# Kernel optimization log

Hardware: AMD Instinct MI355X
Metric: run time of the kernel (lower is better)

The kernel has to match this reference:

```python
import jax, jax.numpy as jnp
import numpy as np

IN_DIM, DIM_MSA, PAIR_DIM = 256, 32, 64
B, L = 1, 512


def setup_inputs() -> dict:
    key = jax.random.key(0)
    k0, k1, k2, k3, k4 = jax.random.split(key, 5)
    seq_rep = jax.random.normal(k0, (B, L, IN_DIM), dtype=jnp.float32)
    # torch nn.Linear params: weight [out, in], bias [out]
    s1 = 1.0 / np.sqrt(IN_DIM)
    W1 = jax.random.uniform(k1, (DIM_MSA, IN_DIM), jnp.float32, -s1, s1)
    b1 = jax.random.uniform(k2, (DIM_MSA,), jnp.float32, -s1, s1)
    s2 = 1.0 / np.sqrt(DIM_MSA * DIM_MSA)
    W2 = jax.random.uniform(k3, (PAIR_DIM, DIM_MSA * DIM_MSA), jnp.float32, -s2, s2)
    b2 = jax.random.uniform(k4, (PAIR_DIM,), jnp.float32, -s2, s2)
    return {"seq_rep": seq_rep, "W1": W1, "b1": b1, "W2": W2, "b2": b2}


def reference(seq_rep, W1, b1, W2, b2):
    # proj_down1: [B,L,in_dim] -> [B,L,dim_msa]
    x = seq_rep @ W1.T + b1
    # outer product: 'bid,bjc -> bijcd' then flatten (c d)
    # [B,L(i),L(j),c(dim_msa),d(dim_msa)]
    outer = jnp.einsum('bid,bjc->bijcd', x, x)
    Bb, Li, Lj = outer.shape[:3]
    outer = outer.reshape(Bb, Li, Lj, DIM_MSA * DIM_MSA)  # (c d), c-major
    # proj_down2: -> [B,L,L,pairwise_dim]
    return outer @ W2.T + b2
```

## Files before the change

### kernel.cpp

```cpp
#include <hip/hip_runtime.h>


static constexpr int LL  = 512;
static constexpr int IND = 256;
static constexpr int DM  = 32;
static constexpr int PD  = 64;

typedef _Float16 f16x4 __attribute__((ext_vector_type(4)));
typedef _Float16 f16x8 __attribute__((ext_vector_type(8)));
typedef float    f32x16 __attribute__((ext_vector_type(16)));

#define LGKM_BARRIER() do { \
    asm volatile("s_waitcnt lgkmcnt(0)" ::: "memory"); \
    __builtin_amdgcn_s_barrier(); \
  } while (0)

__device__ __forceinline__ f16x4 cvt4(const float4 v) {
  f16x4 r;
  r[0] = (_Float16)v.x; r[1] = (_Float16)v.y;
  r[2] = (_Float16)v.z; r[3] = (_Float16)v.w;
  return r;
}

static constexpr int SP = 264;
static constexpr int XP = 40;

__global__ __launch_bounds__(256) void k_front(const float* __restrict__ seq,
                                               const float* __restrict__ W1,
                                               const float* __restrict__ b1,
                                               const float* __restrict__ W2,
                                               _Float16* __restrict__ xgh,
                                               _Float16* __restrict__ Ygh) {
  __shared__ __align__(16) _Float16 seqs[64 * SP];
  __shared__ __align__(16) _Float16 w1s[32 * SP];
  __shared__ __align__(16) _Float16 w2h[64 * XP];
  __shared__ __align__(16) _Float16 xh[64 * XP];
  const int c     = blockIdx.x & 31;
  const int ibase = (blockIdx.x >> 5) * 64;
  const int t     = threadIdx.x;

#pragma unroll
  for (int k = 0; k < 16; ++k) {
    const int f = t + k * 256;
    const int row = f >> 6, c4 = f & 63;
    const float4 v = *(const float4*)(seq + (size_t)(ibase + row) * IND + c4 * 4);
    *(f16x4*)&seqs[row * SP + c4 * 4] = cvt4(v);
  }
#pragma unroll
  for (int k = 0; k < 8; ++k) {
    const int f = t + k * 256;
    const int row = f >> 6, c4 = f & 63;
    const float4 v = *(const float4*)(W1 + (size_t)row * IND + c4 * 4);
    *(f16x4*)&w1s[row * SP + c4 * 4] = cvt4(v);
  }
#pragma unroll
  for (int k = 0; k < 2; ++k) {
    const int idx = t + k * 256;
    const int p = idx >> 3, d4 = idx & 7;
    const float4 v = *(const float4*)(W2 + (size_t)p * (DM * DM) + c * DM + d4 * 4);
    *(f16x4*)&w2h[p * XP + d4 * 4] = cvt4(v);
  }
  __syncthreads();

  const int w = t >> 6, lane = t & 63, l31 = lane & 31, lh = lane >> 5;

  if (w < 2) {
    const _Float16* arow = &seqs[(w * 32 + l31) * SP + lh * 8];
    const _Float16* brow = &w1s[l31 * SP + lh * 8];
    f32x16 acc = {};
#pragma unroll
    for (int ks = 0; ks < 16; ++ks) {
      const f16x8 af = *(const f16x8*)(arow + ks * 16);
      const f16x8 bf = *(const f16x8*)(brow + ks * 16);
      acc = __builtin_amdgcn_mfma_f32_32x32x16_f16(af, bf, acc, 0, 0, 0);
    }
    const float bias1 = b1[l31];
#pragma unroll
    for (int r = 0; r < 16; ++r) {
      const int mrow = w * 32 + (r & 3) + 8 * (r >> 2) + 4 * lh;
      const float v = acc[r] + bias1;
      xh[mrow * XP + l31] = (_Float16)v;
      if (c == 0) xgh[(size_t)(ibase + mrow) * DM + l31] = (_Float16)v;
    }
  }
  __syncthreads();

  {
    const int ih = w >> 1, ph = w & 1;
    const _Float16* arow = &xh[(ih * 32 + l31) * XP + lh * 8];
    const _Float16* brow = &w2h[(ph * 32 + l31) * XP + lh * 8];
    f32x16 acc = {};
    {
      const f16x8 a0 = *(const f16x8*)(arow);
      const f16x8 b0 = *(const f16x8*)(brow);
      acc = __builtin_amdgcn_mfma_f32_32x32x16_f16(a0, b0, acc, 0, 0, 0);
      const f16x8 a1 = *(const f16x8*)(arow + 16);
      const f16x8 b1 = *(const f16x8*)(brow + 16);
      acc = __builtin_amdgcn_mfma_f32_32x32x16_f16(a1, b1, acc, 0, 0, 0);
    }
    _Float16* ybase = Ygh + ((size_t)ibase * DM + c) * PD + ph * 32 + l31;
#pragma unroll
    for (int r = 0; r < 16; ++r) {
      const int irow = ih * 32 + (r & 3) + 8 * (r >> 2) + 4 * lh;
      ybase[(size_t)irow * (DM * PD)] = (_Float16)acc[r];
    }
  }
}

static constexpr int XPAD = 40;

__global__ __launch_bounds__(128, 3) void k_outer(const _Float16* __restrict__ xgh,
                                                  const _Float16* __restrict__ Ygh,
                                                  const float* __restrict__ b2,
                                                  float* __restrict__ out) {
  __shared__ __align__(16) _Float16 xbs[128 * XPAD];
  __shared__ __align__(16) _Float16 ybs[2 * DM * PD];
  __shared__ __align__(16) float    obuf[2][32 * 32];
  const int q  = blockIdx.x & 3;
  const int i0 = blockIdx.x >> 2;
  const int t  = threadIdx.x;

  const int lane = t & 63;
  const int w    = t >> 6;
  const int l31  = lane & 31;
  const int lh   = lane >> 5;
  const int pn   = w * 32 + l31;
  float* const obufW = &obuf[w][0];
  const float4 bias4 = *(const float4*)(b2 + w * 32 + (lane & 7) * 4);

  {
    const f16x8* src = (const f16x8*)(xgh + (size_t)(q * 128 + t) * DM);
    _Float16* dst = &xbs[t * XPAD];
    *(f16x8*)(dst)      = src[0];
    *(f16x8*)(dst + 8)  = src[1];
    *(f16x8*)(dst + 16) = src[2];
    *(f16x8*)(dst + 24) = src[3];
  }
  {
    const f16x8* ys = (const f16x8*)(Ygh + (size_t)i0 * (DM * PD));
    *(f16x8*)&ybs[t * 8]        = ys[t];
    *(f16x8*)&ybs[1024 + t * 8] = ys[128 + t];
  }
  LGKM_BARRIER();

  const f16x8* ys1 = (const f16x8*)(Ygh + (size_t)(i0 + 256) * (DM * PD));
  const f16x8 n0 = ys1[t];
  const f16x8 n1 = ys1[128 + t];

  auto process = [&](int i, const _Float16* __restrict__ yb) {
    f16x8 b0, b1;
#pragma unroll
    for (int e = 0; e < 8; ++e) {
      b0[e] = yb[(lh * 8 + e) * PD + pn];
      b1[e] = yb[(16 + lh * 8 + e) * PD + pn];
    }
    const size_t orow0 = ((size_t)i * LL + q * 128) * PD;
#pragma unroll
    for (int jt = 0; jt < 4; ++jt) {
      const int ai = (jt * 32 + l31) * XPAD + lh * 8;
      const f16x8 a0 = *(const f16x8*)&xbs[ai];
      const f16x8 a1 = *(const f16x8*)&xbs[ai + 16];
      f32x16 acc = {};
      acc = __builtin_amdgcn_mfma_f32_32x32x16_f16(a0, b0, acc, 0, 0, 0);
      acc = __builtin_amdgcn_mfma_f32_32x32x16_f16(a1, b1, acc, 0, 0, 0);
#pragma unroll
      for (int r = 0; r < 16; ++r) {
        const int row = (r & 3) + 8 * (r >> 2) + 4 * lh;
        obufW[row * 32 + l31] = acc[r];
      }
#pragma unroll
      for (int k = 0; k < 4; ++k) {
        const int idx = lane + k * 64;
        const int row = idx >> 3, pseg = idx & 7;
        float4 v = *(const float4*)&obufW[idx * 4];
        v.x += bias4.x; v.y += bias4.y; v.z += bias4.z; v.w += bias4.w;
        *(float4*)(out + orow0 + (size_t)(jt * 32 + row) * PD + w * 32 + pseg * 4) = v;
      }
    }
  };

  process(i0, ybs);

  *(f16x8*)&ybs[2048 + t * 8]        = n0;
  *(f16x8*)&ybs[2048 + 1024 + t * 8] = n1;
  LGKM_BARRIER();

  process(i0 + 256, ybs + 2048);
}

extern "C" void kernel_launch(void* const* d_in, const int* in_sizes, int n_in,
                              void* d_out, int out_size, void* d_ws, size_t ws_size,
                              hipStream_t stream) {
  const float* seq = (const float*)d_in[0];
  const float* W1  = (const float*)d_in[1];
  const float* b1  = (const float*)d_in[2];
  const float* W2  = (const float*)d_in[3];
  const float* b2  = (const float*)d_in[4];
  float* out = (float*)d_out;

  _Float16* xgh = (_Float16*)d_ws;
  _Float16* Ygh = xgh + LL * DM;

  k_front<<<256, 256, 0, stream>>>(seq, W1, b1, W2, xgh, Ygh);
  k_outer<<<LL * 2, 128, 0, stream>>>(xgh, Ygh, b2, out);
}
```

Measured before the change: 22.42 us.

## Fuse front and outer kernels into one persistent launch with a grid-wide atomic barrier

Merges the projection kernel and the outer-product kernel into a single 256-block launch. A global atomic counter acts as a grid barrier between the two phases, and shared memory is reused between them. Each block now handles four i-rows per j-quarter with double-buffered Y tiles, instead of spreading the work over 1024 small blocks. This removes one kernel launch and its inter-kernel gap, but adds a memset, a spin-wait barrier that relies on all 256 blocks being co-resident, and fewer, larger blocks for the output-write phase.

```diff
diff --git a/kernel.cpp b/kernel.cpp
--- a/kernel.cpp
+++ b/kernel.cpp
@@ -24,168 +24,195 @@
 
 static constexpr int SP = 264;
 static constexpr int XP = 40;
-
-__global__ __launch_bounds__(256) void k_front(const float* __restrict__ seq,
+static constexpr int XPAD = 40;
+
+static constexpr int SMEM_BYTES = 60928;
+
+__global__ __launch_bounds__(256) void k_fused(const float* __restrict__ seq,
                                                const float* __restrict__ W1,
                                                const float* __restrict__ b1,
                                                const float* __restrict__ W2,
+                                               const float* __restrict__ b2,
                                                _Float16* __restrict__ xgh,
-                                               _Float16* __restrict__ Ygh) {
-  __shared__ __align__(16) _Float16 seqs[64 * SP];
-  __shared__ __align__(16) _Float16 w1s[32 * SP];
-  __shared__ __align__(16) _Float16 w2h[64 * XP];
-  __shared__ __align__(16) _Float16 xh[64 * XP];
-  const int c     = blockIdx.x & 31;
-  const int ibase = (blockIdx.x >> 5) * 64;
-  const int t     = threadIdx.x;
-
-#pragma unroll
-  for (int k = 0; k < 16; ++k) {
-    const int f = t + k * 256;
-    const int row = f >> 6, c4 = f & 63;
-    const float4 v = *(const float4*)(seq + (size_t)(ibase + row) * IND + c4 * 4);
-    *(f16x4*)&seqs[row * SP + c4 * 4] = cvt4(v);
-  }
-#pragma unroll
-  for (int k = 0; k < 8; ++k) {
-    const int f = t + k * 256;
-    const int row = f >> 6, c4 = f & 63;
-    const float4 v = *(const float4*)(W1 + (size_t)row * IND + c4 * 4);
-    *(f16x4*)&w1s[row * SP + c4 * 4] = cvt4(v);
-  }
-#pragma unroll
-  for (int k = 0; k < 2; ++k) {
-    const int idx = t + k * 256;
-    const int p = idx >> 3, d4 = idx & 7;
-    const float4 v = *(const float4*)(W2 + (size_t)p * (DM * DM) + c * DM + d4 * 4);
-    *(f16x4*)&w2h[p * XP + d4 * 4] = cvt4(v);
-  }
-  __syncthreads();
-
-  const int w = t >> 6, lane = t & 63, l31 = lane & 31, lh = lane >> 5;
-
-  if (w < 2) {
-    const _Float16* arow = &seqs[(w * 32 + l31) * SP + lh * 8];
-    const _Float16* brow = &w1s[l31 * SP + lh * 8];
-    f32x16 acc = {};
-#pragma unroll
-    for (int ks = 0; ks < 16; ++ks) {
-      const f16x8 af = *(const f16x8*)(arow + ks * 16);
-      const f16x8 bf = *(const f16x8*)(brow + ks * 16);
-      acc = __builtin_amdgcn_mfma_f32_32x32x16_f16(af, bf, acc, 0, 0, 0);
-    }
-    const float bias1 = b1[l31];
-#pragma unroll
-    for (int r = 0; r < 16; ++r) {
-      const int mrow = w * 32 + (r & 3) + 8 * (r >> 2) + 4 * lh;
-      const float v = acc[r] + bias1;
-      xh[mrow * XP + l31] = (_Float16)v;
-      if (c == 0) xgh[(size_t)(ibase + mrow) * DM + l31] = (_Float16)v;
-    }
-  }
-  __syncthreads();
+                                               _Float16* __restrict__ Ygh,
+                                               unsigned int* __restrict__ flag,
+                                               float* __restrict__ out) {
+  __shared__ __align__(16) char smem[SMEM_BYTES];
+  const int bid = blockIdx.x;
+  const int t   = threadIdx.x;
+  const int w   = t >> 6, lane = t & 63, l31 = lane & 31, lh = lane >> 5;
 
   {
-    const int ih = w >> 1, ph = w & 1;
-    const _Float16* arow = &xh[(ih * 32 + l31) * XP + lh * 8];
-    const _Float16* brow = &w2h[(ph * 32 + l31) * XP + lh * 8];
-    f32x16 acc = {};
-    {
+    _Float16* seqs = (_Float16*)(smem);
+    _Float16* w1s  = (_Float16*)(smem + 33792);
+    _Float16* w2h  = (_Float16*)(smem + 50688);
+    _Float16* xh   = (_Float16*)(smem + 55808);
+    const int c     = bid & 31;
+    const int ibase = (bid >> 5) * 64;
+
+#pragma unroll
+    for (int k = 0; k < 16; ++k) {
+      const int f = t + k * 256;
+      const int row = f >> 6, c4 = f & 63;
+      const float4 v = *(const float4*)(seq + (size_t)(ibase + row) * IND + c4 * 4);
+      *(f16x4*)&seqs[row * SP + c4 * 4] = cvt4(v);
+    }
+#pragma unroll
+    for (int k = 0; k < 8; ++k) {
+      const int f = t + k * 256;
+      const int row = f >> 6, c4 = f & 63;
+      const float4 v = *(const float4*)(W1 + (size_t)row * IND + c4 * 4);
+      *(f16x4*)&w1s[row * SP + c4 * 4] = cvt4(v);
+    }
+#pragma unroll
+    for (int k = 0; k < 2; ++k) {
+      const int idx = t + k * 256;
+      const int p = idx >> 3, d4 = idx & 7;
+      const float4 v = *(const float4*)(W2 + (size_t)p * (DM * DM) + c * DM + d4 * 4);
+      *(f16x4*)&w2h[p * XP + d4 * 4] = cvt4(v);
+    }
+    __syncthreads();
+
+    if (w < 2) {
+      const _Float16* arow = &seqs[(w * 32 + l31) * SP + lh * 8];
+      const _Float16* brow = &w1s[l31 * SP + lh * 8];
+      f32x16 acc = {};
+#pragma unroll
+      for (int ks = 0; ks < 16; ++ks) {
+        const f16x8 af = *(const f16x8*)(arow + ks * 16);
+        const f16x8 bf = *(const f16x8*)(brow + ks * 16);
+        acc = __builtin_amdgcn_mfma_f32_32x32x16_f16(af, bf, acc, 0, 0, 0);
+      }
+      const float bias1 = b1[l31];
+#pragma unroll
+      for (int r = 0; r < 16; ++r) {
+        const int mrow = w * 32 + (r & 3) + 8 * (r >> 2) + 4 * lh;
+        const float v = acc[r] + bias1;
+        xh[mrow * XP + l31] = (_Float16)v;
+        if (c == 0) xgh[(size_t)(ibase + mrow) * DM + l31] = (_Float16)v;
+      }
+    }
+    __syncthreads();
+
+    {
+      const int ih = w >> 1, ph = w & 1;
+      const _Float16* arow = &xh[(ih * 32 + l31) * XP + lh * 8];
+      const _Float16* brow = &w2h[(ph * 32 + l31) * XP + lh * 8];
+      f32x16 acc = {};
       const f16x8 a0 = *(const f16x8*)(arow);
       const f16x8 b0 = *(const f16x8*)(brow);
       acc = __builtin_amdgcn_mfma_f32_32x32x16_f16(a0, b0, acc, 0, 0, 0);
       const f16x8 a1 = *(const f16x8*)(arow + 16);
-      const f16x8 b1 = *(const f16x8*)(brow + 16);
-      acc = __builtin_amdgcn_mfma_f32_32x32x16_f16(a1, b1, acc, 0, 0, 0);
-    }
-    _Float16* ybase = Ygh + ((size_t)ibase * DM + c) * PD + ph * 32 + l31;
-#pragma unroll
-    for (int r = 0; r < 16; ++r) {
-      const int irow = ih * 32 + (r & 3) + 8 * (r >> 2) + 4 * lh;
-      ybase[(size_t)irow * (DM * PD)] = (_Float16)acc[r];
+      const f16x8 b1f = *(const f16x8*)(brow + 16);
+      acc = __builtin_amdgcn_mfma_f32_32x32x16_f16(a1, b1f, acc, 0, 0, 0);
+      _Float16* ybase = Ygh + ((size_t)ibase * DM + c) * PD + ph * 32 + l31;
+#pragma unroll
+      for (int r = 0; r < 16; ++r) {
+        const int irow = ih * 32 + (r & 3) + 8 * (r >> 2) + 4 * lh;
+        ybase[(size_t)irow * (DM * PD)] = (_Float16)acc[r];
+      }
     }
   }
-}
-
-static constexpr int XPAD = 40;
-
-__global__ __launch_bounds__(128, 3) void k_outer(const _Float16* __restrict__ xgh,
-                                                  const _Float16* __restrict__ Ygh,
-                                                  const float* __restrict__ b2,
-                                                  float* __restrict__ out) {
-  __shared__ __align__(16) _Float16 xbs[128 * XPAD];
-  __shared__ __align__(16) _Float16 ybs[2 * DM * PD];
-  __shared__ __align__(16) float    obuf[2][32 * 32];
-  const int q  = blockIdx.x & 3;
-  const int i0 = blockIdx.x >> 2;
-  const int t  = threadIdx.x;
-
-  const int lane = t & 63;
-  const int w    = t >> 6;
-  const int l31  = lane & 31;
-  const int lh   = lane >> 5;
-  const int pn   = w * 32 + l31;
-  float* const obufW = &obuf[w][0];
-  const float4 bias4 = *(const float4*)(b2 + w * 32 + (lane & 7) * 4);
+
+  __syncthreads();
+  if (t == 0) {
+    __hip_atomic_fetch_add(flag, 1u, __ATOMIC_RELEASE, __HIP_MEMORY_SCOPE_AGENT);
+    while (__hip_atomic_load(flag, __ATOMIC_ACQUIRE, __HIP_MEMORY_SCOPE_AGENT) < 256u)
+      __builtin_amdgcn_s_sleep(8);
+  }
+  __syncthreads();
 
   {
-    const f16x8* src = (const f16x8*)(xgh + (size_t)(q * 128 + t) * DM);
-    _Float16* dst = &xbs[t * XPAD];
-    *(f16x8*)(dst)      = src[0];
-    *(f16x8*)(dst + 8)  = src[1];
-    *(f16x8*)(dst + 16) = src[2];
-    *(f16x8*)(dst + 24) = src[3];
+    _Float16* xbs  = (_Float16*)(smem);
+    _Float16* ybsA = (_Float16*)(smem + 10240);
+    _Float16* ybsB = (_Float16*)(smem + 18432);
+    float*    obuf = (float*)(smem + 26624);
+
+    const int q  = bid & 3;
+    const int i0 = bid >> 2;
+    const int wp = w >> 1;
+    const int ph = w & 1;
+    const int pn = ph * 32 + l31;
+    const int grp = t >> 7;
+    const int tt  = t & 127;
+    float* const obufW = obuf + w * 1024;
+    const float4 bias4 = *(const float4*)(b2 + ph * 32 + (lane & 7) * 4);
+    _Float16* const myYbs = grp ? ybsB : ybsA;
+    const int mybase = i0 + 64 * wp;
+
+    {
+      const int row = t >> 1, half = t & 1;
+      const f16x8* src = (const f16x8*)(xgh + (size_t)(q * 128 + row) * DM + half * 16);
+      _Float16* dst = xbs + row * XPAD + half * 16;
+      *(f16x8*)(dst)     = src[0];
+      *(f16x8*)(dst + 8) = src[1];
+    }
+    {
+      const f16x8* ys = (const f16x8*)(Ygh + (size_t)(i0 + 64 * grp) * (DM * PD));
+      *(f16x8*)&myYbs[tt * 8]        = ys[tt];
+      *(f16x8*)&myYbs[1024 + tt * 8] = ys[128 + tt];
+    }
+    LGKM_BARRIER();
+
+    auto process = [&](int i, const _Float16* __restrict__ yb) {
+      f16x8 bf0, bf1;
+#pragma unroll
+      for (int e = 0; e < 8; ++e) {
+        bf0[e] = yb[(lh * 8 + e) * PD + pn];
+        bf1[e] = yb[(16 + lh * 8 + e) * PD + pn];
+      }
+      const size_t orow0 = ((size_t)i * LL + q * 128) * PD;
+#pragma unroll
+      for (int jt = 0; jt < 4; ++jt) {
+        const int ai = (jt * 32 + l31) * XPAD + lh * 8;
+        const f16x8 a0 = *(const f16x8*)&xbs[ai];
+        const f16x8 a1 = *(const f16x8*)&xbs[ai + 16];
+        f32x16 acc = {};
+        acc = __builtin_amdgcn_mfma_f32_32x32x16_f16(a0, bf0, acc, 0, 0, 0);
+        acc = __builtin_amdgcn_mfma_f32_32x32x16_f16(a1, bf1, acc, 0, 0, 0);
+#pragma unroll
+        for (int r = 0; r < 16; ++r) {
+          const int row = (r & 3) + 8 * (r >> 2) + 4 * lh;
+          obufW[row * 32 + l31] = acc[r];
+        }
+#pragma unroll
+        for (int k = 0; k < 4; ++k) {
+          const int idx = lane + k * 64;
+          const int row = idx >> 3, pseg = idx & 7;
+          float4 v = *(const float4*)&obufW[idx * 4];
+          v.x += bias4.x; v.y += bias4.y; v.z += bias4.z; v.w += bias4.w;
+          *(float4*)(out + orow0 + (size_t)(jt * 32 + row) * PD + ph * 32 + pseg * 4) = v;
+        }
+      }
+    };
+
+    f16x8 n0, n1;
+    {
+      const f16x8* ys = (const f16x8*)(Ygh + (size_t)(mybase + 128) * (DM * PD));
+      n0 = ys[tt]; n1 = ys[128 + tt];
+    }
+    process(mybase, myYbs);
+    *(f16x8*)&myYbs[2048 + tt * 8]        = n0;
+    *(f16x8*)&myYbs[2048 + 1024 + tt * 8] = n1;
+    LGKM_BARRIER();
+    {
+      const f16x8* ys = (const f16x8*)(Ygh + (size_t)(mybase + 256) * (DM * PD));
+      n0 = ys[tt]; n1 = ys[128 + tt];
+    }
+    process(mybase + 128, myYbs + 2048);
+    *(f16x8*)&myYbs[tt * 8]        = n0;
+    *(f16x8*)&myYbs[1024 + tt * 8] = n1;
+    LGKM_BARRIER();
+    {
+      const f16x8* ys = (const f16x8*)(Ygh + (size_t)(mybase + 384) * (DM * PD));
+      n0 = ys[tt]; n1 = ys[128 + tt];
+    }
+    process(mybase + 256, myYbs);
+    *(f16x8*)&myYbs[2048 + tt * 8]        = n0;
+    *(f16x8*)&myYbs[2048 + 1024 + tt * 8] = n1;
+    LGKM_BARRIER();
+    process(mybase + 384, myYbs + 2048);
   }
-  {
-    const f16x8* ys = (const f16x8*)(Ygh + (size_t)i0 * (DM * PD));
-    *(f16x8*)&ybs[t * 8]        = ys[t];
-    *(f16x8*)&ybs[1024 + t * 8] = ys[128 + t];
-  }
-  LGKM_BARRIER();
-
-  const f16x8* ys1 = (const f16x8*)(Ygh + (size_t)(i0 + 256) * (DM * PD));
-  const f16x8 n0 = ys1[t];
-  const f16x8 n1 = ys1[128 + t];
-
-  auto process = [&](int i, const _Float16* __restrict__ yb) {
-    f16x8 b0, b1;
-#pragma unroll
-    for (int e = 0; e < 8; ++e) {
-      b0[e] = yb[(lh * 8 + e) * PD + pn];
-      b1[e] = yb[(16 + lh * 8 + e) * PD + pn];
-    }
-    const size_t orow0 = ((size_t)i * LL + q * 128) * PD;
-#pragma unroll
-    for (int jt = 0; jt < 4; ++jt) {
-      const int ai = (jt * 32 + l31) * XPAD + lh * 8;
-      const f16x8 a0 = *(const f16x8*)&xbs[ai];
-      const f16x8 a1 = *(const f16x8*)&xbs[ai + 16];
-      f32x16 acc = {};
-      acc = __builtin_amdgcn_mfma_f32_32x32x16_f16(a0, b0, acc, 0, 0, 0);
-      acc = __builtin_amdgcn_mfma_f32_32x32x16_f16(a1, b1, acc, 0, 0, 0);
-#pragma unroll
-      for (int r = 0; r < 16; ++r) {
-        const int row = (r & 3) + 8 * (r >> 2) + 4 * lh;
-        obufW[row * 32 + l31] = acc[r];
-      }
-#pragma unroll
-      for (int k = 0; k < 4; ++k) {
-        const int idx = lane + k * 64;
-        const int row = idx >> 3, pseg = idx & 7;
-        float4 v = *(const float4*)&obufW[idx * 4];
-        v.x += bias4.x; v.y += bias4.y; v.z += bias4.z; v.w += bias4.w;
-        *(float4*)(out + orow0 + (size_t)(jt * 32 + row) * PD + w * 32 + pseg * 4) = v;
-      }
-    }
-  };
-
-  process(i0, ybs);
-
-  *(f16x8*)&ybs[2048 + t * 8]        = n0;
-  *(f16x8*)&ybs[2048 + 1024 + t * 8] = n1;
-  LGKM_BARRIER();
-
-  process(i0 + 256, ybs + 2048);
 }
 
 extern "C" void kernel_launch(void* const* d_in, const int* in_sizes, int n_in,
@@ -200,7 +227,9 @@
 
   _Float16* xgh = (_Float16*)d_ws;
   _Float16* Ygh = xgh + LL * DM;
-
-  k_front<<<256, 256, 0, stream>>>(seq, W1, b1, W2, xgh, Ygh);
-  k_outer<<<LL * 2, 128, 0, stream>>>(xgh, Ygh, b2, out);
+  unsigned int* flag = (unsigned int*)((char*)d_ws + (size_t)LL * DM * 2 +
+                                       (size_t)LL * DM * PD * 2);
+
+  hipMemsetAsync(flag, 0, sizeof(unsigned int), stream);
+  k_fused<<<256, 256, 0, stream>>>(seq, W1, b1, W2, b2, xgh, Ygh, flag, out);
 }
```

Measured after the change: 38.47 us. 1.72x slower.
